# Optimization experiments

Hardware: AMD Instinct MI355X
Metric: run time of the kernel (lower is better)

## Reference

```python
import jax, jax.numpy as jnp
import numpy as np

EPS = 1e-6
NUM_HEADS = 16

def _ln(x):
    # LayerNorm32, no affine, eps=1e-6, computed in fp32
    x32 = x.astype(jnp.float32)
    mu = jnp.mean(x32, axis=-1, keepdims=True)
    var = jnp.var(x32, axis=-1, keepdims=True)
    return ((x32 - mu) * jax.lax.rsqrt(var + EPS)).astype(x.dtype)

def _mha(q, k, v):
    # q,k,v: [B, L, H, D]
    d = q.shape[-1]
    scale = 1.0 / jnp.sqrt(jnp.asarray(d, q.dtype))
    s = jnp.einsum('bqhd,bkhd->bhqk', q, k) * scale
    p = jax.nn.softmax(s, axis=-1)
    o = jnp.einsum('bhqk,bkhd->bqhd', p, v)
    return o.reshape(o.shape[0], o.shape[1], -1)

def setup_inputs() -> dict:
    key = jax.random.key(0)
    ks = jax.random.split(key, 10)
    B, L, C, Lc, Cc = 4, 2048, 1024, 1024, 1024
    Dff = 4 * C
    s = 0.02
    return {
        'x': jax.random.normal(ks[0], (B, L, C), jnp.float32),
        'context': jax.random.normal(ks[1], (B, Lc, Cc), jnp.float32),
        'w_qkv': jax.random.normal(ks[2], (C, 3 * C), jnp.float32) * s,
        'b_qkv': jnp.zeros((3 * C,), jnp.float32),
        'w_os': jax.random.normal(ks[3], (C, C), jnp.float32) * s,
        'b_os': jnp.zeros((C,), jnp.float32),
        'w_qc': jax.random.normal(ks[4], (C, C), jnp.float32) * s,
        'b_qc': jnp.zeros((C,), jnp.float32),
        'w_kvc': jax.random.normal(ks[5], (Cc, 2 * C), jnp.float32) * s,
        'b_kvc': jnp.zeros((2 * C,), jnp.float32),
        'w_oc': jax.random.normal(ks[6], (C, C), jnp.float32) * s,
        'b_oc': jnp.zeros((C,), jnp.float32),
        'w_fc1': jax.random.normal(ks[7], (C, Dff), jnp.float32) * s,
        'b_fc1': jnp.zeros((Dff,), jnp.float32),
        'w_fc2': jax.random.normal(ks[8], (Dff, C), jnp.float32) * s,
        'b_fc2': jnp.zeros((C,), jnp.float32),
    }

def reference(x, context, w_qkv, b_qkv, w_os, b_os, w_qc, b_qc, w_kvc, b_kvc,
              w_oc, b_oc, w_fc1, b_fc1, w_fc2, b_fc2):
    B, L, C = x.shape
    H = NUM_HEADS
    D = C // H
    # --- self attention (pre-norm, full) ---
    h = _ln(x)
    qkv = (h @ w_qkv + b_qkv).reshape(B, L, 3, H, D)
    q, k, v = qkv[:, :, 0], qkv[:, :, 1], qkv[:, :, 2]
    h = _mha(q, k, v) @ w_os + b_os
    x = x + h
    # --- cross attention ---
    h = _ln(x)
    q = (h @ w_qc + b_qc).reshape(B, L, H, D)
    Lc = context.shape[1]
    kv = (context @ w_kvc + b_kvc).reshape(B, Lc, 2, H, D)
    k, v = kv[:, :, 0], kv[:, :, 1]
    h = _mha(q, k, v) @ w_oc + b_oc
    x = x + h
    # --- sparse FFN (GELU tanh) ---
    h = _ln(x)
    h = jax.nn.gelu(h @ w_fc1 + b_fc1, approximate=True) @ w_fc2 + b_fc2
    return x + h
```

## Files before the change

kernel.cpp:

```cpp
#include <hip/hip_runtime.h>

typedef unsigned short ushort_t;
typedef __attribute__((ext_vector_type(8))) short short8;
typedef __attribute__((ext_vector_type(4))) float f32x4;
typedef __attribute__((ext_vector_type(4))) unsigned short ushort4v;

__device__ inline ushort_t f2bf(float f) {
    union { float f; unsigned u; } v; v.f = f;
    return (ushort_t)((v.u + 0x7FFFu + ((v.u >> 16) & 1u)) >> 16);
}
__device__ inline float bf2f(ushort_t u) {
    union { unsigned u; float f; } v; v.u = ((unsigned)u) << 16;
    return v.f;
}

__device__ inline void gld16(const ushort_t* g, ushort_t* l) {
    __builtin_amdgcn_global_load_lds(
        (const __attribute__((address_space(1))) unsigned int*)g,
        (__attribute__((address_space(3))) unsigned int*)l, 16, 0, 0);
}

__global__ void w_transpose_bf16(const float* __restrict__ w, ushort_t* __restrict__ out,
                                 int K, int N) {
    __shared__ float t[64][65];
    const int k0 = blockIdx.y * 64, n0 = blockIdx.x * 64;
    const int tid = threadIdx.x;
#pragma unroll
    for (int i = 0; i < 16; i++) {
        int idx = tid + i * 256;
        int r = idx >> 6, c = idx & 63;
        t[r][c] = w[(size_t)(k0 + r) * N + n0 + c];
    }
    __syncthreads();
#pragma unroll
    for (int i = 0; i < 16; i++) {
        int idx = tid + i * 256;
        int nr = idx >> 6, kc = idx & 63;
        out[(size_t)(n0 + nr) * K + k0 + kc] = f2bf(t[kc][nr]);
    }
}

__global__ void v_transpose(const ushort_t* __restrict__ V, int vStride, int rowsPerBatch,
                            ushort_t* __restrict__ Vt, int Lk) {
    __shared__ __align__(16) ushort_t t[64][72];
    const int bh = blockIdx.y, k0 = blockIdx.x * 64;
    const int b = bh >> 4, h = bh & 15;
    const int tid = threadIdx.x;
    const ushort_t* src = V + (size_t)(b * rowsPerBatch + k0) * vStride + h * 64;
#pragma unroll
    for (int i = 0; i < 2; i++) {
        int ch = tid + i * 256;
        int r = ch >> 3, c = (ch & 7) * 8;
        *(short8*)(&t[r][c]) = *(const short8*)(src + (size_t)r * vStride + c);
    }
    __syncthreads();
#pragma unroll
    for (int i = 0; i < 2; i++) {
        int ch = tid + i * 256;
        int d = ch >> 3, c = (ch & 7) * 8;
        short8 o;
#pragma unroll
        for (int j = 0; j < 8; j++) o[j] = (short)t[c + j][d];
        *(short8*)(Vt + ((size_t)bh * 64 + d) * Lk + k0 + c) = o;
    }
}

__global__ void f32_to_bf16_vec(const float* __restrict__ in, ushort_t* __restrict__ out, int n4) {
    int i = blockIdx.x * blockDim.x + threadIdx.x;
    if (i < n4) {
        float4 v = ((const float4*)in)[i];
        ushort4v o;
        o[0] = f2bf(v.x); o[1] = f2bf(v.y); o[2] = f2bf(v.z); o[3] = f2bf(v.w);
        ((ushort4v*)out)[i] = o;
    }
}

__global__ void ln_rows(const float* __restrict__ in, ushort_t* __restrict__ out) {
    __shared__ float s1[4], s2[4];
    const int row = blockIdx.x;
    const int tid = threadIdx.x;
    const float4 v = ((const float4*)(in + (size_t)row * 1024))[tid];
    float s  = v.x + v.y + v.z + v.w;
    float ss = v.x * v.x + v.y * v.y + v.z * v.z + v.w * v.w;
#pragma unroll
    for (int d = 32; d >= 1; d >>= 1) {
        s  += __shfl_down(s, d, 64);
        ss += __shfl_down(ss, d, 64);
    }
    if ((tid & 63) == 0) { s1[tid >> 6] = s; s2[tid >> 6] = ss; }
    __syncthreads();
    float sum = s1[0] + s1[1] + s1[2] + s1[3];
    float sqs = s2[0] + s2[1] + s2[2] + s2[3];
    float mu  = sum * (1.0f / 1024.0f);
    float var = sqs * (1.0f / 1024.0f) - mu * mu;
    float rs  = rsqrtf(var + 1e-6f);
    ushort4v o;
    o[0] = f2bf((v.x - mu) * rs);
    o[1] = f2bf((v.y - mu) * rs);
    o[2] = f2bf((v.z - mu) * rs);
    o[3] = f2bf((v.w - mu) * rs);
    ((ushort4v*)(out + (size_t)row * 1024))[tid] = o;
}

#define EPI_BF16 0
#define EPI_GELU 1
#define EPI_RES  2

template <int EPI>
__global__ void gemm_bt(const ushort_t* __restrict__ A, const ushort_t* __restrict__ Bt,
                        const float* __restrict__ bias, const float* __restrict__ res,
                        void* __restrict__ outp, int M, int N, int K) {
    __shared__ __align__(16) ushort_t As[128 * 64];
    __shared__ __align__(16) ushort_t Bs[128 * 64];
    const int tid = threadIdx.x;
    const int lane = tid & 63, wave = tid >> 6;
    const int m0 = blockIdx.y * 128, n0 = blockIdx.x * 128;
    const int wr = (wave >> 1) * 64, wc = (wave & 1) * 64;
    const int lr = lane & 15, lg = lane >> 4;

    f32x4 acc[4][4];
#pragma unroll
    for (int i = 0; i < 4; i++)
#pragma unroll
        for (int j = 0; j < 4; j++) acc[i][j] = f32x4{0.f, 0.f, 0.f, 0.f};

    for (int k0 = 0; k0 < K; k0 += 64) {
#pragma unroll
        for (int i = 0; i < 4; i++) {
            int ch = tid + i * 256;
            int r = ch >> 3;
            int kcs = (((ch & 7) ^ (r & 7))) * 8;
            gld16(A  + (size_t)(m0 + r) * K + k0 + kcs, As + ch * 8);
            gld16(Bt + (size_t)(n0 + r) * K + k0 + kcs, Bs + ch * 8);
        }
        __syncthreads();
#pragma unroll
        for (int ks = 0; ks < 2; ks++) {
            short8 af[4], bfr[4];
#pragma unroll
            for (int m = 0; m < 4; m++) {
                int r = wr + m * 16 + lr;
                int kc = ks * 4 + lg;
                af[m] = *(const short8*)(As + r * 64 + ((kc ^ (r & 7)) << 3));
            }
#pragma unroll
            for (int n = 0; n < 4; n++) {
                int r = wc + n * 16 + lr;
                int kc = ks * 4 + lg;
                bfr[n] = *(const short8*)(Bs + r * 64 + ((kc ^ (r & 7)) << 3));
            }
#pragma unroll
            for (int m = 0; m < 4; m++)
#pragma unroll
                for (int n = 0; n < 4; n++)
                    acc[m][n] = __builtin_amdgcn_mfma_f32_16x16x32_bf16(af[m], bfr[n], acc[m][n], 0, 0, 0);
        }
        __syncthreads();
    }

#pragma unroll
    for (int m = 0; m < 4; m++) {
        int rowb = m0 + wr + m * 16 + lg * 4;
#pragma unroll
        for (int n = 0; n < 4; n++) {
            int col = n0 + wc + n * 16 + lr;
            float bcol = bias[col];
            f32x4 v = acc[m][n];
#pragma unroll
            for (int q = 0; q < 4; q++) {
                float x = v[q] + bcol;
                if (EPI == EPI_GELU) {
                    float u = 0.7978845608028654f * (x + 0.044715f * x * x * x);
                    x = 0.5f * x * (1.0f + tanhf(u));
                }
                size_t off = (size_t)(rowb + q) * N + col;
                if (EPI == EPI_RES) ((float*)outp)[off] = x + res[off];
                else                ((ushort_t*)outp)[off] = f2bf(x);
            }
        }
    }
}

__global__ void attn_fwd(const ushort_t* __restrict__ Q, int qStride,
                         const ushort_t* __restrict__ Kp, int kvStride, int kvBatchRows,
                         const ushort_t* __restrict__ Vt, int Lk,
                         ushort_t* __restrict__ O) {
    __shared__ __align__(16) ushort_t Ks[2][64 * 64];
    __shared__ __align__(16) ushort_t Vts[2][64 * 64];
    __shared__ __align__(16) ushort_t Ps[4][16 * 64];
    const int tid = threadIdx.x, lane = tid & 63, wave = tid >> 6;
    const int lr = lane & 15, lg = lane >> 4;
    const int b = blockIdx.z, h = blockIdx.y, qb = blockIdx.x;
    const int qRow0 = b * 2048 + qb * 64;
    const int kvRow0 = b * kvBatchRows;
    const int hc = h * 64;
    const ushort_t* vt_base = Vt + (size_t)(b * 16 + h) * 64 * Lk;

    short8 qf[2];
    {
        const ushort_t* qrow = Q + (size_t)(qRow0 + wave * 16 + lr) * qStride + hc;
        short8 r0 = *(const short8*)(qrow + lg * 8);
        short8 r1 = *(const short8*)(qrow + 32 + lg * 8);
#pragma unroll
        for (int j = 0; j < 8; j++) {
            qf[0][j] = (short)f2bf(bf2f((ushort_t)r0[j]) * 0.125f);
            qf[1][j] = (short)f2bf(bf2f((ushort_t)r1[j]) * 0.125f);
        }
    }

    f32x4 oacc[4];
#pragma unroll
    for (int d = 0; d < 4; d++) oacc[d] = f32x4{0.f, 0.f, 0.f, 0.f};
    float mrun = -INFINITY, lrun = 0.f;

    const int nt = Lk >> 6;

    auto stage = [&](int buf, int kt) {
#pragma unroll
        for (int i = 0; i < 2; i++) {
            int ch = tid + i * 256;
            int r = ch >> 3;
            int kcs = (((ch & 7) ^ (r & 7))) * 8;
            gld16(Kp + (size_t)(kvRow0 + kt + r) * kvStride + hc + kcs, Ks[buf] + ch * 8);
            gld16(vt_base + (size_t)r * Lk + kt + kcs, Vts[buf] + ch * 8);
        }
    };

    stage(0, 0);
    __syncthreads();
    int cur = 0;

    for (int t = 0; t < nt; ++t) {
        if (t + 1 < nt) stage(cur ^ 1, (t + 1) * 64);

        const ushort_t* Kc = Ks[cur];
        const ushort_t* Vc = Vts[cur];

        f32x4 sacc[4];
#pragma unroll
        for (int n = 0; n < 4; n++) {
            int r = n * 16 + lr;
            short8 k0 = *(const short8*)(Kc + r * 64 + ((lg ^ (r & 7)) << 3));
            short8 k1 = *(const short8*)(Kc + r * 64 + (((4 + lg) ^ (r & 7)) << 3));
            f32x4 s = f32x4{0.f, 0.f, 0.f, 0.f};
            s = __builtin_amdgcn_mfma_f32_16x16x32_bf16(k0, qf[0], s, 0, 0, 0);
            s = __builtin_amdgcn_mfma_f32_16x16x32_bf16(k1, qf[1], s, 0, 0, 0);
            sacc[n] = s;
        }

        float mx = sacc[0][0];
#pragma unroll
        for (int n = 0; n < 4; n++)
#pragma unroll
            for (int r = 0; r < 4; r++) if (n | r) mx = fmaxf(mx, sacc[n][r]);
        mx = fmaxf(mx, __shfl_xor(mx, 16, 64));
        mx = fmaxf(mx, __shfl_xor(mx, 32, 64));

        if (!__all(mx <= mrun + 8.0f)) {
            float mnew = fmaxf(mrun, mx);
            float al = __expf(mrun - mnew);
            float a0 = __shfl(al, lg * 4 + 0, 64);
            float a1 = __shfl(al, lg * 4 + 1, 64);
            float a2 = __shfl(al, lg * 4 + 2, 64);
            float a3 = __shfl(al, lg * 4 + 3, 64);
#pragma unroll
            for (int dn = 0; dn < 4; dn++) {
                oacc[dn][0] *= a0; oacc[dn][1] *= a1;
                oacc[dn][2] *= a2; oacc[dn][3] *= a3;
            }
            lrun *= al;
            mrun = mnew;
        }

        float rsum = 0.f;
#pragma unroll
        for (int n = 0; n < 4; n++)
#pragma unroll
            for (int r = 0; r < 4; r++) {
                float p = __expf(sacc[n][r] - mrun);
                sacc[n][r] = p;
                rsum += p;
            }
        rsum += __shfl_xor(rsum, 16, 64);
        rsum += __shfl_xor(rsum, 32, 64);
        lrun += rsum;

        ushort_t* Pw = &Ps[wave][0];
#pragma unroll
        for (int n = 0; n < 4; n++) {
            unsigned w0, w1;
            asm("v_cvt_pk_bf16_f32 %0, %1, %2" : "=v"(w0) : "v"(sacc[n][0]), "v"(sacc[n][1]));
            asm("v_cvt_pk_bf16_f32 %0, %1, %2" : "=v"(w1) : "v"(sacc[n][2]), "v"(sacc[n][3]));
            int kc = n * 2 + (lg >> 1);
            uint2 u; u.x = w0; u.y = w1;
            *(uint2*)((char*)Pw + lr * 128 + ((kc ^ (lr & 7)) << 4) + (lg & 1) * 8) = u;
        }

        short8 pf0 = *(const short8*)(Pw + lr * 64 + ((lg ^ (lr & 7)) << 3));
        short8 pf1 = *(const short8*)(Pw + lr * 64 + (((4 + lg) ^ (lr & 7)) << 3));
#pragma unroll
        for (int dn = 0; dn < 4; dn++) {
            int r = dn * 16 + lr;
            short8 v0 = *(const short8*)(Vc + r * 64 + ((lg ^ (r & 7)) << 3));
            short8 v1 = *(const short8*)(Vc + r * 64 + (((4 + lg) ^ (r & 7)) << 3));
            oacc[dn] = __builtin_amdgcn_mfma_f32_16x16x32_bf16(pf0, v0, oacc[dn], 0, 0, 0);
            oacc[dn] = __builtin_amdgcn_mfma_f32_16x16x32_bf16(pf1, v1, oacc[dn], 0, 0, 0);
        }
        __syncthreads();
        cur ^= 1;
    }

    float linv[4];
#pragma unroll
    for (int r = 0; r < 4; r++) linv[r] = 1.0f / __shfl(lrun, lg * 4 + r, 64);

#pragma unroll
    for (int dn = 0; dn < 4; dn++)
#pragma unroll
        for (int q = 0; q < 4; q++) {
            float o = oacc[dn][q] * linv[q];
            int row = qRow0 + wave * 16 + lg * 4 + q;
            int col = hc + dn * 16 + lr;
            O[(size_t)row * 1024 + col] = f2bf(o);
        }
}

extern "C" void kernel_launch(void* const* d_in, const int* in_sizes, int n_in,
                              void* d_out, int out_size, void* d_ws, size_t ws_size,
                              hipStream_t stream) {
    const float* x     = (const float*)d_in[0];
    const float* ctx   = (const float*)d_in[1];
    const float* w_qkv = (const float*)d_in[2];
    const float* b_qkv = (const float*)d_in[3];
    const float* w_os  = (const float*)d_in[4];
    const float* b_os  = (const float*)d_in[5];
    const float* w_qc  = (const float*)d_in[6];
    const float* b_qc  = (const float*)d_in[7];
    const float* w_kvc = (const float*)d_in[8];
    const float* b_kvc = (const float*)d_in[9];
    const float* w_oc  = (const float*)d_in[10];
    const float* b_oc  = (const float*)d_in[11];
    const float* w_fc1 = (const float*)d_in[12];
    const float* b_fc1 = (const float*)d_in[13];
    const float* w_fc2 = (const float*)d_in[14];
    const float* b_fc2 = (const float*)d_in[15];
    float* out = (float*)d_out;

    char* ws = (char*)d_ws;
    ushort_t* wqkvT = (ushort_t*)(ws + 0);
    ushort_t* wosT  = (ushort_t*)(ws + 6291456);
    ushort_t* wqcT  = (ushort_t*)(ws + 8388608);
    ushort_t* wkvcT = (ushort_t*)(ws + 10485760);
    ushort_t* wocT  = (ushort_t*)(ws + 14680064);
    ushort_t* wfc1T = (ushort_t*)(ws + 16777216);
    ushort_t* wfc2T = (ushort_t*)(ws + 25165824);
    ushort_t* qkv_bf  = (ushort_t*)(ws + 33554432);
    ushort_t* q_bf    = (ushort_t*)(ws + 33554432);
    ushort_t* kv_bf   = (ushort_t*)(ws + 50331648);
    ushort_t* vt_c    = (ushort_t*)(ws + 67108864);
    ushort_t* ffn_bf  = (ushort_t*)(ws + 33554432);
    ushort_t* ctx_bf  = (ushort_t*)(ws + 83886080);
    ushort_t* attn_bf = (ushort_t*)(ws + 92274688);
    ushort_t* h_bf    = (ushort_t*)(ws + 109051904);
    ushort_t* vt_s    = (ushort_t*)(ws + 109051904);

    const dim3 tb(256);
    w_transpose_bf16<<<dim3(48, 16), tb, 0, stream>>>(w_qkv, wqkvT, 1024, 3072);
    w_transpose_bf16<<<dim3(16, 16), tb, 0, stream>>>(w_os,  wosT,  1024, 1024);
    w_transpose_bf16<<<dim3(16, 16), tb, 0, stream>>>(w_qc,  wqcT,  1024, 1024);
    w_transpose_bf16<<<dim3(32, 16), tb, 0, stream>>>(w_kvc, wkvcT, 1024, 2048);
    w_transpose_bf16<<<dim3(16, 16), tb, 0, stream>>>(w_oc,  wocT,  1024, 1024);
    w_transpose_bf16<<<dim3(64, 16), tb, 0, stream>>>(w_fc1, wfc1T, 1024, 4096);
    w_transpose_bf16<<<dim3(16, 64), tb, 0, stream>>>(w_fc2, wfc2T, 4096, 1024);
    f32_to_bf16_vec<<<4096, tb, 0, stream>>>(ctx, ctx_bf, 1048576);

    ln_rows<<<8192, tb, 0, stream>>>(x, h_bf);
    gemm_bt<EPI_BF16><<<dim3(24, 64), tb, 0, stream>>>(h_bf, wqkvT, b_qkv, nullptr, qkv_bf, 8192, 3072, 1024);
    v_transpose<<<dim3(32, 64), tb, 0, stream>>>(qkv_bf + 2048, 3072, 2048, vt_s, 2048);
    attn_fwd<<<dim3(32, 16, 4), tb, 0, stream>>>(qkv_bf, 3072, qkv_bf + 1024, 3072, 2048,
                                                 vt_s, 2048, attn_bf);
    gemm_bt<EPI_RES><<<dim3(8, 64), tb, 0, stream>>>(attn_bf, wosT, b_os, x, out, 8192, 1024, 1024);

    ln_rows<<<8192, tb, 0, stream>>>(out, h_bf);
    gemm_bt<EPI_BF16><<<dim3(8, 64), tb, 0, stream>>>(h_bf, wqcT, b_qc, nullptr, q_bf, 8192, 1024, 1024);
    gemm_bt<EPI_BF16><<<dim3(16, 32), tb, 0, stream>>>(ctx_bf, wkvcT, b_kvc, nullptr, kv_bf, 4096, 2048, 1024);
    v_transpose<<<dim3(16, 64), tb, 0, stream>>>(kv_bf + 1024, 2048, 1024, vt_c, 1024);
    attn_fwd<<<dim3(32, 16, 4), tb, 0, stream>>>(q_bf, 1024, kv_bf, 2048, 1024,
                                                 vt_c, 1024, attn_bf);
    gemm_bt<EPI_RES><<<dim3(8, 64), tb, 0, stream>>>(attn_bf, wocT, b_oc, out, out, 8192, 1024, 1024);

    ln_rows<<<8192, tb, 0, stream>>>(out, h_bf);
    gemm_bt<EPI_GELU><<<dim3(32, 64), tb, 0, stream>>>(h_bf, wfc1T, b_fc1, nullptr, ffn_bf, 8192, 4096, 1024);
    gemm_bt<EPI_RES><<<dim3(8, 64), tb, 0, stream>>>(ffn_bf, wfc2T, b_fc2, out, out, 8192, 1024, 4096);
}
```

Measured before the change: 614.9 us.

## Add 256x256 eight-wave GEMM and widen attention blocks to 512 threads

Adds a new 256x256-tile GEMM kernel with 8 waves, double-buffered LDS, staggered B-half prefetch, barrier-interleaved MFMA phases and s_setprio. It is used for the QKV and FC1 projections. The attention kernel now runs 8 waves per block over 128 query rows, so each staged K/V tile is shared by twice as many waves, and its MFMA sections are wrapped in s_setprio. The goal is more data reuse per tile and better overlap of loads with matrix math, at the cost of higher register and LDS pressure per block.

```diff
diff --git a/kernel.cpp b/kernel.cpp
--- a/kernel.cpp
+++ b/kernel.cpp
@@ -181,17 +181,170 @@
     }
 }
 
-__global__ void attn_fwd(const ushort_t* __restrict__ Q, int qStride,
-                         const ushort_t* __restrict__ Kp, int kvStride, int kvBatchRows,
-                         const ushort_t* __restrict__ Vt, int Lk,
-                         ushort_t* __restrict__ O) {
+template <int EPI>
+__global__ __launch_bounds__(512, 2)
+void gemm256_bt(const ushort_t* __restrict__ A, const ushort_t* __restrict__ Bt,
+                const float* __restrict__ bias,
+                void* __restrict__ outp, int M, int N, int K) {
+    __shared__ __align__(16) ushort_t As[2][256 * 64];
+    __shared__ __align__(16) ushort_t Bs[2][256 * 64];
+    const int tid = threadIdx.x;
+    const int lane = tid & 63, wave = tid >> 6;
+    const int wm = wave >> 2, wn = wave & 3;
+    const int lr = lane & 15, lg = lane >> 4;
+    const int m0 = blockIdx.y * 256, n0 = blockIdx.x * 256;
+    const int nkt = K >> 6;
+
+    f32x4 acc[8][4];
+#pragma unroll
+    for (int i = 0; i < 8; i++)
+#pragma unroll
+        for (int j = 0; j < 4; j++) acc[i][j] = f32x4{0.f, 0.f, 0.f, 0.f};
+
+#define STAGE_A(buf, kt)                                                        \
+    do {                                                                        \
+        _Pragma("unroll")                                                       \
+        for (int i_ = 0; i_ < 4; i_++) {                                        \
+            int ch_ = tid + i_ * 512;                                           \
+            int r_ = ch_ >> 3;                                                  \
+            int c_ = (((ch_ & 7) ^ (r_ & 7))) << 3;                             \
+            gld16(A + (size_t)(m0 + r_) * K + (kt) + c_, &As[buf][ch_ * 8]);    \
+        }                                                                       \
+    } while (0)
+
+#define STAGE_BH(buf, kt, half)                                                 \
+    do {                                                                        \
+        _Pragma("unroll")                                                       \
+        for (int i_ = 0; i_ < 2; i_++) {                                        \
+            int ch_ = tid + i_ * 512;                                           \
+            int r_ = (half) * 128 + (ch_ >> 3);                                 \
+            int c_ = (((ch_ & 7) ^ (r_ & 7))) << 3;                             \
+            gld16(Bt + (size_t)(n0 + r_) * K + (kt) + c_,                       \
+                  &Bs[buf][(half) * 8192 + ch_ * 8]);                           \
+        }                                                                       \
+    } while (0)
+
+#define RD_A(buf, mf, ks)                                                       \
+    (*(const short8*)(&As[buf][(wm * 128 + (mf) * 16 + lr) * 64 +               \
+        ((((ks) * 4 + lg) ^ ((wm * 128 + (mf) * 16 + lr) & 7)) << 3)]))
+#define RD_B(buf, nf, ks)                                                       \
+    (*(const short8*)(&Bs[buf][(wn * 64 + (nf) * 16 + lr) * 64 +                \
+        ((((ks) * 4 + lg) ^ ((wn * 64 + (nf) * 16 + lr) & 7)) << 3)]))
+
+#define QUAD(MB)                                                                \
+    do {                                                                        \
+        _Pragma("unroll")                                                       \
+        for (int nf_ = 0; nf_ < 4; nf_++) {                                     \
+            acc[MB][nf_]     = __builtin_amdgcn_mfma_f32_16x16x32_bf16(         \
+                aq0, bfr[nf_][0], acc[MB][nf_], 0, 0, 0);                       \
+            acc[MB][nf_]     = __builtin_amdgcn_mfma_f32_16x16x32_bf16(         \
+                aq1, bfr[nf_][1], acc[MB][nf_], 0, 0, 0);                       \
+            acc[MB + 1][nf_] = __builtin_amdgcn_mfma_f32_16x16x32_bf16(         \
+                aq2, bfr[nf_][0], acc[MB + 1][nf_], 0, 0, 0);                   \
+            acc[MB + 1][nf_] = __builtin_amdgcn_mfma_f32_16x16x32_bf16(         \
+                aq3, bfr[nf_][1], acc[MB + 1][nf_], 0, 0, 0);                   \
+        }                                                                       \
+    } while (0)
+
+    STAGE_A(0, 0);
+    STAGE_BH(0, 0, 0); STAGE_BH(0, 0, 1);
+    if (nkt > 1) {
+        STAGE_BH(1, 64, 0); STAGE_BH(1, 64, 1);
+        asm volatile("s_waitcnt vmcnt(4)" ::: "memory");
+    } else {
+        asm volatile("s_waitcnt vmcnt(0)" ::: "memory");
+    }
+    __builtin_amdgcn_s_barrier();
+
+    for (int t = 0; t < nkt; ++t) {
+        const int b = t & 1;
+        short8 bfr[4][2];
+#pragma unroll
+        for (int nf = 0; nf < 4; nf++) {
+            bfr[nf][0] = RD_B(b, nf, 0);
+            bfr[nf][1] = RD_B(b, nf, 1);
+        }
+        {
+            short8 aq0 = RD_A(b, 0, 0), aq1 = RD_A(b, 0, 1);
+            short8 aq2 = RD_A(b, 1, 0), aq3 = RD_A(b, 1, 1);
+            if (t + 1 < nkt) STAGE_A(b ^ 1, (t + 1) << 6);
+            __builtin_amdgcn_s_barrier();
+            __builtin_amdgcn_s_setprio(1);
+            QUAD(0);
+            __builtin_amdgcn_s_setprio(0);
+            __builtin_amdgcn_s_barrier();
+        }
+        {
+            short8 aq0 = RD_A(b, 2, 0), aq1 = RD_A(b, 2, 1);
+            short8 aq2 = RD_A(b, 3, 0), aq3 = RD_A(b, 3, 1);
+            if (t + 2 < nkt) STAGE_BH(b, (t + 2) << 6, 0);
+            __builtin_amdgcn_s_barrier();
+            __builtin_amdgcn_s_setprio(1);
+            QUAD(2);
+            __builtin_amdgcn_s_setprio(0);
+            __builtin_amdgcn_s_barrier();
+        }
+        {
+            short8 aq0 = RD_A(b, 4, 0), aq1 = RD_A(b, 4, 1);
+            short8 aq2 = RD_A(b, 5, 0), aq3 = RD_A(b, 5, 1);
+            if (t + 2 < nkt) STAGE_BH(b, (t + 2) << 6, 1);
+            __builtin_amdgcn_s_barrier();
+            __builtin_amdgcn_s_setprio(1);
+            QUAD(4);
+            __builtin_amdgcn_s_setprio(0);
+            __builtin_amdgcn_s_barrier();
+        }
+        {
+            short8 aq0 = RD_A(b, 6, 0), aq1 = RD_A(b, 6, 1);
+            short8 aq2 = RD_A(b, 7, 0), aq3 = RD_A(b, 7, 1);
+            __builtin_amdgcn_s_barrier();
+            __builtin_amdgcn_s_setprio(1);
+            QUAD(6);
+            __builtin_amdgcn_s_setprio(0);
+            if (t + 2 < nkt)      asm volatile("s_waitcnt vmcnt(4)" ::: "memory");
+            else if (t + 1 < nkt) asm volatile("s_waitcnt vmcnt(0)" ::: "memory");
+            __builtin_amdgcn_s_barrier();
+        }
+    }
+
+#pragma unroll
+    for (int mf = 0; mf < 8; mf++) {
+        int rowb = m0 + wm * 128 + mf * 16 + lg * 4;
+#pragma unroll
+        for (int nf = 0; nf < 4; nf++) {
+            int col = n0 + wn * 64 + nf * 16 + lr;
+            float bcol = bias[col];
+            f32x4 v = acc[mf][nf];
+#pragma unroll
+            for (int q = 0; q < 4; q++) {
+                float x = v[q] + bcol;
+                if (EPI == EPI_GELU) {
+                    float u = 0.7978845608028654f * (x + 0.044715f * x * x * x);
+                    x = 0.5f * x * (1.0f + tanhf(u));
+                }
+                ((ushort_t*)outp)[(size_t)(rowb + q) * N + col] = f2bf(x);
+            }
+        }
+    }
+#undef STAGE_A
+#undef STAGE_BH
+#undef RD_A
+#undef RD_B
+#undef QUAD
+}
+
+__global__ __launch_bounds__(512, 2)
+void attn_fwd(const ushort_t* __restrict__ Q, int qStride,
+              const ushort_t* __restrict__ Kp, int kvStride, int kvBatchRows,
+              const ushort_t* __restrict__ Vt, int Lk,
+              ushort_t* __restrict__ O) {
     __shared__ __align__(16) ushort_t Ks[2][64 * 64];
     __shared__ __align__(16) ushort_t Vts[2][64 * 64];
-    __shared__ __align__(16) ushort_t Ps[4][16 * 64];
+    __shared__ __align__(16) ushort_t Ps[8][16 * 64];
     const int tid = threadIdx.x, lane = tid & 63, wave = tid >> 6;
     const int lr = lane & 15, lg = lane >> 4;
     const int b = blockIdx.z, h = blockIdx.y, qb = blockIdx.x;
-    const int qRow0 = b * 2048 + qb * 64;
+    const int qRow0 = b * 2048 + qb * 128;
     const int kvRow0 = b * kvBatchRows;
     const int hc = h * 64;
     const ushort_t* vt_base = Vt + (size_t)(b * 16 + h) * 64 * Lk;
@@ -216,14 +369,10 @@
     const int nt = Lk >> 6;
 
     auto stage = [&](int buf, int kt) {
-#pragma unroll
-        for (int i = 0; i < 2; i++) {
-            int ch = tid + i * 256;
-            int r = ch >> 3;
-            int kcs = (((ch & 7) ^ (r & 7))) * 8;
-            gld16(Kp + (size_t)(kvRow0 + kt + r) * kvStride + hc + kcs, Ks[buf] + ch * 8);
-            gld16(vt_base + (size_t)r * Lk + kt + kcs, Vts[buf] + ch * 8);
-        }
+        int r = tid >> 3;
+        int kcs = (((tid & 7) ^ (r & 7))) * 8;
+        gld16(Kp + (size_t)(kvRow0 + kt + r) * kvStride + hc + kcs, Ks[buf] + tid * 8);
+        gld16(vt_base + (size_t)r * Lk + kt + kcs, Vts[buf] + tid * 8);
     };
 
     stage(0, 0);
@@ -237,6 +386,7 @@
         const ushort_t* Vc = Vts[cur];
 
         f32x4 sacc[4];
+        __builtin_amdgcn_s_setprio(1);
 #pragma unroll
         for (int n = 0; n < 4; n++) {
             int r = n * 16 + lr;
@@ -247,6 +397,7 @@
             s = __builtin_amdgcn_mfma_f32_16x16x32_bf16(k1, qf[1], s, 0, 0, 0);
             sacc[n] = s;
         }
+        __builtin_amdgcn_s_setprio(0);
 
         float mx = sacc[0][0];
 #pragma unroll
@@ -298,6 +449,7 @@
 
         short8 pf0 = *(const short8*)(Pw + lr * 64 + ((lg ^ (lr & 7)) << 3));
         short8 pf1 = *(const short8*)(Pw + lr * 64 + (((4 + lg) ^ (lr & 7)) << 3));
+        __builtin_amdgcn_s_setprio(1);
 #pragma unroll
         for (int dn = 0; dn < 4; dn++) {
             int r = dn * 16 + lr;
@@ -306,6 +458,7 @@
             oacc[dn] = __builtin_amdgcn_mfma_f32_16x16x32_bf16(pf0, v0, oacc[dn], 0, 0, 0);
             oacc[dn] = __builtin_amdgcn_mfma_f32_16x16x32_bf16(pf1, v1, oacc[dn], 0, 0, 0);
         }
+        __builtin_amdgcn_s_setprio(0);
         __syncthreads();
         cur ^= 1;
     }
@@ -365,6 +518,7 @@
     ushort_t* vt_s    = (ushort_t*)(ws + 109051904);
 
     const dim3 tb(256);
+    const dim3 tb512(512);
     w_transpose_bf16<<<dim3(48, 16), tb, 0, stream>>>(w_qkv, wqkvT, 1024, 3072);
     w_transpose_bf16<<<dim3(16, 16), tb, 0, stream>>>(w_os,  wosT,  1024, 1024);
     w_transpose_bf16<<<dim3(16, 16), tb, 0, stream>>>(w_qc,  wqcT,  1024, 1024);
@@ -375,21 +529,21 @@
     f32_to_bf16_vec<<<4096, tb, 0, stream>>>(ctx, ctx_bf, 1048576);
 
     ln_rows<<<8192, tb, 0, stream>>>(x, h_bf);
-    gemm_bt<EPI_BF16><<<dim3(24, 64), tb, 0, stream>>>(h_bf, wqkvT, b_qkv, nullptr, qkv_bf, 8192, 3072, 1024);
+    gemm256_bt<EPI_BF16><<<dim3(12, 32), tb512, 0, stream>>>(h_bf, wqkvT, b_qkv, qkv_bf, 8192, 3072, 1024);
     v_transpose<<<dim3(32, 64), tb, 0, stream>>>(qkv_bf + 2048, 3072, 2048, vt_s, 2048);
-    attn_fwd<<<dim3(32, 16, 4), tb, 0, stream>>>(qkv_bf, 3072, qkv_bf + 1024, 3072, 2048,
-                                                 vt_s, 2048, attn_bf);
+    attn_fwd<<<dim3(16, 16, 4), tb512, 0, stream>>>(qkv_bf, 3072, qkv_bf + 1024, 3072, 2048,
+                                                    vt_s, 2048, attn_bf);
     gemm_bt<EPI_RES><<<dim3(8, 64), tb, 0, stream>>>(attn_bf, wosT, b_os, x, out, 8192, 1024, 1024);
 
     ln_rows<<<8192, tb, 0, stream>>>(out, h_bf);
     gemm_bt<EPI_BF16><<<dim3(8, 64), tb, 0, stream>>>(h_bf, wqcT, b_qc, nullptr, q_bf, 8192, 1024, 1024);
     gemm_bt<EPI_BF16><<<dim3(16, 32), tb, 0, stream>>>(ctx_bf, wkvcT, b_kvc, nullptr, kv_bf, 4096, 2048, 1024);
     v_transpose<<<dim3(16, 64), tb, 0, stream>>>(kv_bf + 1024, 2048, 1024, vt_c, 1024);
-    attn_fwd<<<dim3(32, 16, 4), tb, 0, stream>>>(q_bf, 1024, kv_bf, 2048, 1024,
-                                                 vt_c, 1024, attn_bf);
+    attn_fwd<<<dim3(16, 16, 4), tb512, 0, stream>>>(q_bf, 1024, kv_bf, 2048, 1024,
+                                                    vt_c, 1024, attn_bf);
     gemm_bt<EPI_RES><<<dim3(8, 64), tb, 0, stream>>>(attn_bf, wocT, b_oc, out, out, 8192, 1024, 1024);
 
     ln_rows<<<8192, tb, 0, stream>>>(out, h_bf);
-    gemm_bt<EPI_GELU><<<dim3(32, 64), tb, 0, stream>>>(h_bf, wfc1T, b_fc1, nullptr, ffn_bf, 8192, 4096, 1024);
+    gemm256_bt<EPI_GELU><<<dim3(16, 32), tb512, 0, stream>>>(h_bf, wfc1T, b_fc1, ffn_bf, 8192, 4096, 1024);
     gemm_bt<EPI_RES><<<dim3(8, 64), tb, 0, stream>>>(ffn_bf, wfc2T, b_fc2, out, out, 8192, 1024, 4096);
 }
```

Result: no change. 622.9 us (+1.3%).

## Enlarge attention blocks to 128 queries, add XCD swizzle and MFMA priority

Applied to the files above, without the earlier changes.

The attention kernel now runs 512 threads (8 waves) per block covering 128 query rows, so each staged K/V tile is shared by twice as many queries. It uses a 1D grid with an XCD-aware swizzle so blocks of the same head and batch land on the same XCD. The GEMM also remaps block IDs with the XCD swizzle to improve L2 locality. s_setprio raises wave priority around the MFMA sections. Risks include reduced occupancy from the larger blocks, and the swizzle assumes the grid size divides evenly by 8.

```diff
diff --git a/kernel.cpp b/kernel.cpp
--- a/kernel.cpp
+++ b/kernel.cpp
@@ -18,6 +18,11 @@
     __builtin_amdgcn_global_load_lds(
         (const __attribute__((address_space(1))) unsigned int*)g,
         (__attribute__((address_space(3))) unsigned int*)l, 16, 0, 0);
+}
+
+__device__ inline int xcd_swz(int id, int nwg) {
+    int q = nwg >> 3;
+    return (id & 7) * q + (id >> 3);
 }
 
 __global__ void w_transpose_bf16(const float* __restrict__ w, ushort_t* __restrict__ out,
@@ -114,7 +119,9 @@
     __shared__ __align__(16) ushort_t Bs[128 * 64];
     const int tid = threadIdx.x;
     const int lane = tid & 63, wave = tid >> 6;
-    const int m0 = blockIdx.y * 128, n0 = blockIdx.x * 128;
+    const int nwg = gridDim.x * gridDim.y;
+    const int sid = xcd_swz(blockIdx.y * gridDim.x + blockIdx.x, nwg);
+    const int m0 = (sid / gridDim.x) * 128, n0 = (sid % gridDim.x) * 128;
     const int wr = (wave >> 1) * 64, wc = (wave & 1) * 64;
     const int lr = lane & 15, lg = lane >> 4;
 
@@ -181,17 +188,19 @@
     }
 }
 
-__global__ void attn_fwd(const ushort_t* __restrict__ Q, int qStride,
-                         const ushort_t* __restrict__ Kp, int kvStride, int kvBatchRows,
-                         const ushort_t* __restrict__ Vt, int Lk,
-                         ushort_t* __restrict__ O) {
+__global__ __launch_bounds__(512, 2)
+void attn_fwd(const ushort_t* __restrict__ Q, int qStride,
+              const ushort_t* __restrict__ Kp, int kvStride, int kvBatchRows,
+              const ushort_t* __restrict__ Vt, int Lk,
+              ushort_t* __restrict__ O) {
     __shared__ __align__(16) ushort_t Ks[2][64 * 64];
     __shared__ __align__(16) ushort_t Vts[2][64 * 64];
-    __shared__ __align__(16) ushort_t Ps[4][16 * 64];
+    __shared__ __align__(16) ushort_t Ps[8][16 * 64];
     const int tid = threadIdx.x, lane = tid & 63, wave = tid >> 6;
     const int lr = lane & 15, lg = lane >> 4;
-    const int b = blockIdx.z, h = blockIdx.y, qb = blockIdx.x;
-    const int qRow0 = b * 2048 + qb * 64;
+    const int sid = xcd_swz(blockIdx.x, gridDim.x);
+    const int qb = sid & 15, h = (sid >> 4) & 15, b = sid >> 8;
+    const int qRow0 = b * 2048 + qb * 128;
     const int kvRow0 = b * kvBatchRows;
     const int hc = h * 64;
     const ushort_t* vt_base = Vt + (size_t)(b * 16 + h) * 64 * Lk;
@@ -216,14 +225,10 @@
     const int nt = Lk >> 6;
 
     auto stage = [&](int buf, int kt) {
-#pragma unroll
-        for (int i = 0; i < 2; i++) {
-            int ch = tid + i * 256;
-            int r = ch >> 3;
-            int kcs = (((ch & 7) ^ (r & 7))) * 8;
-            gld16(Kp + (size_t)(kvRow0 + kt + r) * kvStride + hc + kcs, Ks[buf] + ch * 8);
-            gld16(vt_base + (size_t)r * Lk + kt + kcs, Vts[buf] + ch * 8);
-        }
+        int r = tid >> 3;
+        int kcs = (((tid & 7) ^ (r & 7))) * 8;
+        gld16(Kp + (size_t)(kvRow0 + kt + r) * kvStride + hc + kcs, Ks[buf] + tid * 8);
+        gld16(vt_base + (size_t)r * Lk + kt + kcs, Vts[buf] + tid * 8);
     };
 
     stage(0, 0);
@@ -237,6 +242,7 @@
         const ushort_t* Vc = Vts[cur];
 
         f32x4 sacc[4];
+        __builtin_amdgcn_s_setprio(1);
 #pragma unroll
         for (int n = 0; n < 4; n++) {
             int r = n * 16 + lr;
@@ -247,6 +253,7 @@
             s = __builtin_amdgcn_mfma_f32_16x16x32_bf16(k1, qf[1], s, 0, 0, 0);
             sacc[n] = s;
         }
+        __builtin_amdgcn_s_setprio(0);
 
         float mx = sacc[0][0];
 #pragma unroll
@@ -298,6 +305,7 @@
 
         short8 pf0 = *(const short8*)(Pw + lr * 64 + ((lg ^ (lr & 7)) << 3));
         short8 pf1 = *(const short8*)(Pw + lr * 64 + (((4 + lg) ^ (lr & 7)) << 3));
+        __builtin_amdgcn_s_setprio(1);
 #pragma unroll
         for (int dn = 0; dn < 4; dn++) {
             int r = dn * 16 + lr;
@@ -306,6 +314,7 @@
             oacc[dn] = __builtin_amdgcn_mfma_f32_16x16x32_bf16(pf0, v0, oacc[dn], 0, 0, 0);
             oacc[dn] = __builtin_amdgcn_mfma_f32_16x16x32_bf16(pf1, v1, oacc[dn], 0, 0, 0);
         }
+        __builtin_amdgcn_s_setprio(0);
         __syncthreads();
         cur ^= 1;
     }
@@ -365,6 +374,7 @@
     ushort_t* vt_s    = (ushort_t*)(ws + 109051904);
 
     const dim3 tb(256);
+    const dim3 tb512(512);
     w_transpose_bf16<<<dim3(48, 16), tb, 0, stream>>>(w_qkv, wqkvT, 1024, 3072);
     w_transpose_bf16<<<dim3(16, 16), tb, 0, stream>>>(w_os,  wosT,  1024, 1024);
     w_transpose_bf16<<<dim3(16, 16), tb, 0, stream>>>(w_qc,  wqcT,  1024, 1024);
@@ -377,16 +387,16 @@
     ln_rows<<<8192, tb, 0, stream>>>(x, h_bf);
     gemm_bt<EPI_BF16><<<dim3(24, 64), tb, 0, stream>>>(h_bf, wqkvT, b_qkv, nullptr, qkv_bf, 8192, 3072, 1024);
     v_transpose<<<dim3(32, 64), tb, 0, stream>>>(qkv_bf + 2048, 3072, 2048, vt_s, 2048);
-    attn_fwd<<<dim3(32, 16, 4), tb, 0, stream>>>(qkv_bf, 3072, qkv_bf + 1024, 3072, 2048,
-                                                 vt_s, 2048, attn_bf);
+    attn_fwd<<<dim3(1024), tb512, 0, stream>>>(qkv_bf, 3072, qkv_bf + 1024, 3072, 2048,
+                                               vt_s, 2048, attn_bf);
     gemm_bt<EPI_RES><<<dim3(8, 64), tb, 0, stream>>>(attn_bf, wosT, b_os, x, out, 8192, 1024, 1024);
 
     ln_rows<<<8192, tb, 0, stream>>>(out, h_bf);
     gemm_bt<EPI_BF16><<<dim3(8, 64), tb, 0, stream>>>(h_bf, wqcT, b_qc, nullptr, q_bf, 8192, 1024, 1024);
     gemm_bt<EPI_BF16><<<dim3(16, 32), tb, 0, stream>>>(ctx_bf, wkvcT, b_kvc, nullptr, kv_bf, 4096, 2048, 1024);
     v_transpose<<<dim3(16, 64), tb, 0, stream>>>(kv_bf + 1024, 2048, 1024, vt_c, 1024);
-    attn_fwd<<<dim3(32, 16, 4), tb, 0, stream>>>(q_bf, 1024, kv_bf, 2048, 1024,
-                                                 vt_c, 1024, attn_bf);
+    attn_fwd<<<dim3(1024), tb512, 0, stream>>>(q_bf, 1024, kv_bf, 2048, 1024,
+                                               vt_c, 1024, attn_bf);
     gemm_bt<EPI_RES><<<dim3(8, 64), tb, 0, stream>>>(attn_bf, wocT, b_oc, out, out, 8192, 1024, 1024);
 
     ln_rows<<<8192, tb, 0, stream>>>(out, h_bf);
```

Measured after the change: 589.6 us. -4.1%, faster.
